# Kernel optimization log

Measured on AMD Instinct MI355X. Metric: run time of the kernel, lower is better.

Reference implementation:

```python
import jax, jax.numpy as jnp
import numpy as np

N_RAYS = 8192
N_SAMPLES = 512  # hardcoded n_samples=512 in source
HID = 32
BOOSTER = 1.0


def setup_inputs() -> dict:
    key = jax.random.key(0)
    ks = jax.random.split(key, 8)
    # camera placed outside the box at z=-3, rays pointing toward +z into the aabb
    o = jnp.array([0.0, 0.0, -3.0]) + 0.05 * jax.random.normal(ks[0], (N_RAYS, 3))
    dxy = 0.5 * (2.0 * jax.random.uniform(ks[1], (N_RAYS, 2)) - 1.0)
    d = jnp.concatenate([dxy, jnp.ones((N_RAYS, 1))], axis=-1)  # unnormalized world dirs
    aabb = jnp.array([[-1.0, -1.0, -1.0], [1.0, 1.0, 1.0]])
    u = jax.random.uniform(ks[2], (N_RAYS, N_SAMPLES))  # stratified jitter
    W1 = 0.5 * jax.random.normal(ks[3], (3, HID))
    b1 = jnp.zeros((HID,))
    Wc = 0.2 * jax.random.normal(ks[4], (HID, 3))
    bc = jnp.zeros((3,))
    Wd = 0.2 * jax.random.normal(ks[5], (HID, 1))
    bd = jnp.zeros((1,))
    return dict(o=o, d=d, aabb=aabb, u=u, W1=W1, b1=b1, Wc=Wc, bc=bc, Wd=Wd, bd=bd)


def reference(o, d, aabb, u, W1, b1, Wc, bc, Wd, bd):
    # --- intersect_aabb (slab test) ---
    t1 = (aabb[0] - o) / d
    t2 = (aabb[1] - o) / d
    tnear = jnp.maximum(jnp.max(jnp.minimum(t1, t2), axis=-1), 0.0)  # [N]
    tfar = jnp.min(jnp.maximum(t1, t2), axis=-1)                      # [N]
    active = tnear < tfar                                             # [N] active_mask
    dnorm = jnp.linalg.norm(d, axis=-1, keepdims=True)                # [N,1]

    # --- sample_ray_step_stratified: T bins in [tnear, tfar], jittered ---
    idx = jnp.arange(N_SAMPLES, dtype=o.dtype)
    ts = tnear[:, None] + (tfar - tnear)[:, None] * (idx[None, :] + u) / N_SAMPLES  # [N,T]

    # --- query radiance field at xyz = o + d*ts ---
    xyz = o[:, None, :] + d[:, None, :] * ts[..., None]               # [N,T,3]
    ndc = 2.0 * (xyz - aabb[0]) / (aabb[1] - aabb[0]) - 1.0           # box-normalized
    inbox = jnp.all(jnp.abs(ndc) <= 1.0, axis=-1)                     # BoundsFilter.test
    h = jax.nn.relu(ndc @ W1 + b1)                                    # [N,T,HID]
    color = jax.nn.sigmoid(h @ Wc + bc)                               # [N,T,3]
    density = jax.nn.softplus(h @ Wd + bd)[..., 0]                    # [N,T]
    # masked scatter-back: out-of-box samples contribute zero
    density = jnp.where(inbox, density, 0.0)
    color = jnp.where(inbox[..., None], color, 0.0)

    # --- integrate_timesteps: alpha compositing with cumulative transmittance ---
    t_ext = jnp.concatenate([ts, (tfar + BOOSTER)[:, None]], axis=-1)
    delta = (t_ext[:, 1:] - t_ext[:, :-1]) * dnorm                    # [N,T]
    sd = density * delta
    trans = jnp.exp(-jnp.concatenate([jnp.zeros_like(sd[:, :1]), jnp.cumsum(sd[:, :-1], axis=-1)], axis=-1))
    w = trans * (1.0 - jnp.exp(-sd))                                  # weights [N,T]

    out_color = jnp.einsum('nt,ntc->nc', w, color)                    # color_map
    out_alpha = jnp.sum(w, axis=-1, keepdims=True)                    # alpha_map

    act = active[:, None].astype(o.dtype)                             # scatter to active rays only
    return jnp.concatenate([out_color * act, out_alpha * act], axis=-1)  # [N,4]
```

## Files before the change

kernel.cpp:

```cpp
#include <hip/hip_runtime.h>
#include <math.h>

#define NRAYS 8192
#define NS 512
#define HID 32
#define SPL 4

typedef float f32x2 __attribute__((ext_vector_type(2)));

__global__ __launch_bounds__(256) void render_kernel(
    const float* __restrict__ o_, const float* __restrict__ d_,
    const float* __restrict__ aabb, const float* __restrict__ u_,
    const float* __restrict__ W1, const float* __restrict__ b1,
    const float* __restrict__ Wc, const float* __restrict__ bc,
    const float* __restrict__ Wd, const float* __restrict__ bd,
    float* __restrict__ out)
{
    __shared__ float wsh[260];
    __shared__ float wtot[2][2];
    __shared__ float4 wpart[2][2];
    const int tid = threadIdx.x;

    if (tid < HID) {
        const int j = tid;
        float* base = wsh + j * 8;
        base[0] = W1[0 * HID + j];
        base[1] = W1[1 * HID + j];
        base[2] = W1[2 * HID + j];
        base[3] = b1[j];
        base[4] = Wc[j * 3 + 0];
        base[5] = Wc[j * 3 + 1];
        base[6] = Wc[j * 3 + 2];
        base[7] = Wd[j];
    } else if (tid == HID) {
        wsh[256] = bc[0]; wsh[257] = bc[1]; wsh[258] = bc[2]; wsh[259] = bd[0];
    }
    __syncthreads();

    const int lane = tid & 63;
    const int wave = tid >> 6;
    const int pair = wave >> 1;
    const int half = wave & 1;
    const int ray  = (blockIdx.x << 1) + pair;

    const float ox = o_[ray * 3 + 0], oy = o_[ray * 3 + 1], oz = o_[ray * 3 + 2];
    const float dx = d_[ray * 3 + 0], dy = d_[ray * 3 + 1], dz = d_[ray * 3 + 2];
    const float lox = aabb[0], loy = aabb[1], loz = aabb[2];
    const float hix = aabb[3], hiy = aabb[4], hiz = aabb[5];

    float t1 = (lox - ox) / dx, t2 = (hix - ox) / dx;
    float tnear = fminf(t1, t2), tfar = fmaxf(t1, t2);
    t1 = (loy - oy) / dy; t2 = (hiy - oy) / dy;
    tnear = fmaxf(tnear, fminf(t1, t2)); tfar = fminf(tfar, fmaxf(t1, t2));
    t1 = (loz - oz) / dz; t2 = (hiz - oz) / dz;
    tnear = fmaxf(tnear, fminf(t1, t2)); tfar = fminf(tfar, fmaxf(t1, t2));
    tnear = fmaxf(tnear, 0.0f);

    const bool active = (tnear < tfar);

    float sd[SPL], csum[SPL], colR[SPL], colG[SPL], colB[SPL];
    float Lsc = 0.0f, cum = 0.0f, T = 0.0f;

    if (active) {
        const float dnorm = sqrtf(dx * dx + dy * dy + dz * dz);
        const float dt = (tfar - tnear) * (1.0f / (float)NS);
        const float sx = 2.0f / (hix - lox);
        const float sy = 2.0f / (hiy - loy);
        const float sz = 2.0f / (hiz - loz);
        const float bc0 = wsh[256], bc1 = wsh[257], bc2 = wsh[258], bd0 = wsh[259];

        const float cx = (ox - lox) * sx - 1.0f, gx = dx * sx;
        const float cy = (oy - loy) * sy - 1.0f, gy = dy * sy;
        const float cz = (oz - loz) * sz - 1.0f, gz = dz * sz;

        const int t0 = (half << 8) + (lane << 2);
        const float* __restrict__ urow = u_ + (size_t)ray * NS;
        const float4 ua = *reinterpret_cast<const float4*>(urow + t0);
        const float unext = (t0 + 4 < NS) ? urow[t0 + 4] : 0.0f;
        float us[5] = {ua.x, ua.y, ua.z, ua.w, unext};

        float tsv[SPL], delta[SPL];
        #pragma unroll
        for (int s = 0; s < SPL; ++s) {
            const int t = t0 + s;
            tsv[s] = fmaf(dt, (float)t + us[s], tnear);
            const float dl = (t == NS - 1) ? (tfar + 1.0f) - tsv[s]
                                           : dt * (1.0f + us[s + 1] - us[s]);
            delta[s] = dl * dnorm;
        }
        const f32x2 ts01 = {tsv[0], tsv[1]};
        const f32x2 ts23 = {tsv[2], tsv[3]};

        f32x2 cr01 = {bc0, bc0}, cr23 = {bc0, bc0};
        f32x2 cg01 = {bc1, bc1}, cg23 = {bc1, bc1};
        f32x2 cb01 = {bc2, bc2}, cb23 = {bc2, bc2};
        f32x2 dd01 = {bd0, bd0}, dd23 = {bd0, bd0};

        const float4* __restrict__ wq = reinterpret_cast<const float4*>(wsh);
        #pragma unroll 4
        for (int j = 0; j < HID; ++j) {
            const float4 qa = wq[j * 2 + 0];
            const float4 qb = wq[j * 2 + 1];
            const float A = fmaf(cx, qa.x, fmaf(cy, qa.y, fmaf(cz, qa.z, qa.w)));
            const float B = fmaf(gx, qa.x, fmaf(gy, qa.y, gz * qa.z));
            const f32x2 A2 = {A, A}, B2 = {B, B};
            f32x2 h01 = __builtin_elementwise_max(
                __builtin_elementwise_fma(ts01, B2, A2), (f32x2){0.0f, 0.0f});
            f32x2 h23 = __builtin_elementwise_max(
                __builtin_elementwise_fma(ts23, B2, A2), (f32x2){0.0f, 0.0f});
            const f32x2 wr = {qb.x, qb.x}, wg = {qb.y, qb.y};
            const f32x2 wb = {qb.z, qb.z}, wd2 = {qb.w, qb.w};
            cr01 = __builtin_elementwise_fma(h01, wr, cr01);
            cr23 = __builtin_elementwise_fma(h23, wr, cr23);
            cg01 = __builtin_elementwise_fma(h01, wg, cg01);
            cg23 = __builtin_elementwise_fma(h23, wg, cg23);
            cb01 = __builtin_elementwise_fma(h01, wb, cb01);
            cb23 = __builtin_elementwise_fma(h23, wb, cb23);
            dd01 = __builtin_elementwise_fma(h01, wd2, dd01);
            dd23 = __builtin_elementwise_fma(h23, wd2, dd23);
        }

        const float ddv[SPL] = {dd01.x, dd01.y, dd23.x, dd23.y};
        const float crv[SPL] = {cr01.x, cr01.y, cr23.x, cr23.y};
        const float cgv[SPL] = {cg01.x, cg01.y, cg23.x, cg23.y};
        const float cbv[SPL] = {cb01.x, cb01.y, cb23.x, cb23.y};

        cum = 0.0f;
        #pragma unroll
        for (int s = 0; s < SPL; ++s) {
            const float dd = ddv[s];
            const float dens = fmaxf(dd, 0.0f) + __logf(1.0f + __expf(-fabsf(dd)));
            sd[s] = dens * delta[s];
            cum += sd[s];
            csum[s] = cum;
            colR[s] = __builtin_amdgcn_rcpf(1.0f + __expf(-crv[s]));
            colG[s] = __builtin_amdgcn_rcpf(1.0f + __expf(-cgv[s]));
            colB[s] = __builtin_amdgcn_rcpf(1.0f + __expf(-cbv[s]));
        }

        Lsc = cum;
        #pragma unroll
        for (int off = 1; off < 64; off <<= 1) {
            const float v = __shfl_up(Lsc, off);
            Lsc += (lane >= off) ? v : 0.0f;
        }
        T = __shfl(Lsc, 63);
    }

    if (lane == 0) wtot[pair][half] = T;
    __syncthreads();

    float4 partial = make_float4(0.0f, 0.0f, 0.0f, 0.0f);
    if (active) {
        const float E = (half ? wtot[pair][0] : 0.0f) + (Lsc - cum);
        const float e0 = __expf(-E);
        float eprev = e0;
        float aR = 0.0f, aG = 0.0f, aB = 0.0f;
        #pragma unroll
        for (int s = 0; s < SPL; ++s) {
            const float ecur = __expf(-(E + csum[s]));
            const float w = eprev - ecur;
            eprev = ecur;
            aR = fmaf(w, colR[s], aR);
            aG = fmaf(w, colG[s], aG);
            aB = fmaf(w, colB[s], aB);
        }
        float aA = e0 - eprev;

        #pragma unroll
        for (int off = 32; off; off >>= 1) {
            aR += __shfl_xor(aR, off);
            aG += __shfl_xor(aG, off);
            aB += __shfl_xor(aB, off);
            aA += __shfl_xor(aA, off);
        }
        partial = make_float4(aR, aG, aB, aA);
    }

    if (lane == 0) wpart[pair][half] = partial;
    __syncthreads();

    if (half == 0 && lane == 0) {
        const float4 p0 = wpart[pair][0];
        const float4 p1 = wpart[pair][1];
        reinterpret_cast<float4*>(out)[ray] =
            make_float4(p0.x + p1.x, p0.y + p1.y, p0.z + p1.z, p0.w + p1.w);
    }
}

extern "C" void kernel_launch(void* const* d_in, const int* in_sizes, int n_in,
                              void* d_out, int out_size, void* d_ws, size_t ws_size,
                              hipStream_t stream) {
    const float* o_   = (const float*)d_in[0];
    const float* d_   = (const float*)d_in[1];
    const float* aabb = (const float*)d_in[2];
    const float* u_   = (const float*)d_in[3];
    const float* W1   = (const float*)d_in[4];
    const float* b1   = (const float*)d_in[5];
    const float* Wc   = (const float*)d_in[6];
    const float* bc   = (const float*)d_in[7];
    const float* Wd   = (const float*)d_in[8];
    const float* bd   = (const float*)d_in[9];
    float* out = (float*)d_out;

    render_kernel<<<NRAYS / 2, 256, 0, stream>>>(o_, d_, aabb, u_, W1, b1, Wc, bc, Wd, bd, out);
}
```

Before: 111.2 us.

## Keep MLP weights in registers and broadcast via readlane instead of LDS

Drops the shared-memory staging of the MLP weights and the block barrier that followed it. Each lane now loads the weights for hidden unit j = lane&31 and precomputes that unit's per-ray affine terms A and B. The hidden loop then broadcasts them with readlane into scalar registers, which removes the per-iteration LDS reads and the redundant per-sample recomputation of A and B. The loop is fully unrolled and launch bounds now request occupancy, at the cost of 32×6 readlane instructions and possible register pressure.

```diff
diff --git a/kernel.cpp b/kernel.cpp
--- a/kernel.cpp
+++ b/kernel.cpp
@@ -8,7 +8,7 @@
 
 typedef float f32x2 __attribute__((ext_vector_type(2)));
 
-__global__ __launch_bounds__(256) void render_kernel(
+__global__ __launch_bounds__(256, 8) void render_kernel(
     const float* __restrict__ o_, const float* __restrict__ d_,
     const float* __restrict__ aabb, const float* __restrict__ u_,
     const float* __restrict__ W1, const float* __restrict__ b1,
@@ -16,32 +16,26 @@
     const float* __restrict__ Wd, const float* __restrict__ bd,
     float* __restrict__ out)
 {
-    __shared__ float wsh[260];
     __shared__ float wtot[2][2];
     __shared__ float4 wpart[2][2];
-    const int tid = threadIdx.x;
-
-    if (tid < HID) {
-        const int j = tid;
-        float* base = wsh + j * 8;
-        base[0] = W1[0 * HID + j];
-        base[1] = W1[1 * HID + j];
-        base[2] = W1[2 * HID + j];
-        base[3] = b1[j];
-        base[4] = Wc[j * 3 + 0];
-        base[5] = Wc[j * 3 + 1];
-        base[6] = Wc[j * 3 + 2];
-        base[7] = Wd[j];
-    } else if (tid == HID) {
-        wsh[256] = bc[0]; wsh[257] = bc[1]; wsh[258] = bc[2]; wsh[259] = bd[0];
-    }
-    __syncthreads();
-
+
+    const int tid  = threadIdx.x;
     const int lane = tid & 63;
     const int wave = tid >> 6;
     const int pair = wave >> 1;
     const int half = wave & 1;
     const int ray  = (blockIdx.x << 1) + pair;
+
+    const int j0 = lane & 31;
+    const float w1x = W1[0 * HID + j0];
+    const float w1y = W1[1 * HID + j0];
+    const float w1z = W1[2 * HID + j0];
+    const float b1j = b1[j0];
+    const float wrj = Wc[j0 * 3 + 0];
+    const float wgj = Wc[j0 * 3 + 1];
+    const float wbj = Wc[j0 * 3 + 2];
+    const float wdj = Wd[j0];
+    const float bc0 = bc[0], bc1 = bc[1], bc2 = bc[2], bd0 = bd[0];
 
     const float ox = o_[ray * 3 + 0], oy = o_[ray * 3 + 1], oz = o_[ray * 3 + 2];
     const float dx = d_[ray * 3 + 0], dy = d_[ray * 3 + 1], dz = d_[ray * 3 + 2];
@@ -67,11 +61,12 @@
         const float sx = 2.0f / (hix - lox);
         const float sy = 2.0f / (hiy - loy);
         const float sz = 2.0f / (hiz - loz);
-        const float bc0 = wsh[256], bc1 = wsh[257], bc2 = wsh[258], bd0 = wsh[259];
 
         const float cx = (ox - lox) * sx - 1.0f, gx = dx * sx;
         const float cy = (oy - loy) * sy - 1.0f, gy = dy * sy;
         const float cz = (oz - loz) * sz - 1.0f, gz = dz * sz;
+        const float Av = fmaf(cx, w1x, fmaf(cy, w1y, fmaf(cz, w1z, b1j)));
+        const float Bv = fmaf(gx, w1x, fmaf(gy, w1y, gz * w1z));
 
         const int t0 = (half << 8) + (lane << 2);
         const float* __restrict__ urow = u_ + (size_t)ray * NS;
@@ -96,28 +91,27 @@
         f32x2 cb01 = {bc2, bc2}, cb23 = {bc2, bc2};
         f32x2 dd01 = {bd0, bd0}, dd23 = {bd0, bd0};
 
-        const float4* __restrict__ wq = reinterpret_cast<const float4*>(wsh);
-        #pragma unroll 4
+        #pragma unroll
         for (int j = 0; j < HID; ++j) {
-            const float4 qa = wq[j * 2 + 0];
-            const float4 qb = wq[j * 2 + 1];
-            const float A = fmaf(cx, qa.x, fmaf(cy, qa.y, fmaf(cz, qa.z, qa.w)));
-            const float B = fmaf(gx, qa.x, fmaf(gy, qa.y, gz * qa.z));
-            const f32x2 A2 = {A, A}, B2 = {B, B};
-            f32x2 h01 = __builtin_elementwise_max(
+            const float Aj = __int_as_float(__builtin_amdgcn_readlane(__float_as_int(Av), j));
+            const float Bj = __int_as_float(__builtin_amdgcn_readlane(__float_as_int(Bv), j));
+            const float wr = __int_as_float(__builtin_amdgcn_readlane(__float_as_int(wrj), j));
+            const float wg = __int_as_float(__builtin_amdgcn_readlane(__float_as_int(wgj), j));
+            const float wb = __int_as_float(__builtin_amdgcn_readlane(__float_as_int(wbj), j));
+            const float wd = __int_as_float(__builtin_amdgcn_readlane(__float_as_int(wdj), j));
+            const f32x2 A2 = {Aj, Aj}, B2 = {Bj, Bj};
+            const f32x2 h01 = __builtin_elementwise_max(
                 __builtin_elementwise_fma(ts01, B2, A2), (f32x2){0.0f, 0.0f});
-            f32x2 h23 = __builtin_elementwise_max(
+            const f32x2 h23 = __builtin_elementwise_max(
                 __builtin_elementwise_fma(ts23, B2, A2), (f32x2){0.0f, 0.0f});
-            const f32x2 wr = {qb.x, qb.x}, wg = {qb.y, qb.y};
-            const f32x2 wb = {qb.z, qb.z}, wd2 = {qb.w, qb.w};
-            cr01 = __builtin_elementwise_fma(h01, wr, cr01);
-            cr23 = __builtin_elementwise_fma(h23, wr, cr23);
-            cg01 = __builtin_elementwise_fma(h01, wg, cg01);
-            cg23 = __builtin_elementwise_fma(h23, wg, cg23);
-            cb01 = __builtin_elementwise_fma(h01, wb, cb01);
-            cb23 = __builtin_elementwise_fma(h23, wb, cb23);
-            dd01 = __builtin_elementwise_fma(h01, wd2, dd01);
-            dd23 = __builtin_elementwise_fma(h23, wd2, dd23);
+            cr01 = __builtin_elementwise_fma(h01, (f32x2){wr, wr}, cr01);
+            cr23 = __builtin_elementwise_fma(h23, (f32x2){wr, wr}, cr23);
+            cg01 = __builtin_elementwise_fma(h01, (f32x2){wg, wg}, cg01);
+            cg23 = __builtin_elementwise_fma(h23, (f32x2){wg, wg}, cg23);
+            cb01 = __builtin_elementwise_fma(h01, (f32x2){wb, wb}, cb01);
+            cb23 = __builtin_elementwise_fma(h23, (f32x2){wb, wb}, cb23);
+            dd01 = __builtin_elementwise_fma(h01, (f32x2){wd, wd}, dd01);
+            dd23 = __builtin_elementwise_fma(h23, (f32x2){wd, wd}, dd23);
         }
 
         const float ddv[SPL] = {dd01.x, dd01.y, dd23.x, dd23.y};
```

Result: no change. 112.8 us (+1.5%).
